# Kernel optimization log

Measured on AMD Instinct MI355X. Metric: run time of the kernel, lower is better.

Reference implementation:

```python
import jax, jax.numpy as jnp
import numpy as np

V = 50000      # word vocab
CV = 63        # char vocab (60 chars + 3 tags)
HW = 512       # word hidden size
HC = 256       # char hidden size
NLW = 2        # word lstm layers
NLC = 2        # char lstm layers
L = 12         # chars in the word


def _lstm_layers(x, H, C, Wih, Whh, bih, bhh):
    """One time-step of a multi-layer LSTM (PyTorch gate order i,f,g,o).
    x: [1, D], H/C: [nl, 1, D]. Returns (top_h, newH, newC)."""
    nl = Wih.shape[0]
    newH, newC = [], []
    inp = x
    for l in range(nl):
        gates = inp @ Wih[l].T + H[l] @ Whh[l].T + bih[l] + bhh[l]  # [1, 4D]
        i, f, g, o = jnp.split(gates, 4, axis=-1)
        i = jax.nn.sigmoid(i)
        f = jax.nn.sigmoid(f)
        g = jnp.tanh(g)
        o = jax.nn.sigmoid(o)
        c = f * C[l] + i * g
        h = o * jnp.tanh(c)
        newH.append(h)
        newC.append(c)
        inp = h
    return inp, jnp.stack(newH), jnp.stack(newC)


def setup_inputs() -> dict:
    key = jax.random.key(0)
    ks = jax.random.split(key, 20)
    sW = 1.0 / np.sqrt(HW)
    sC = 1.0 / np.sqrt(HC)
    return {
        "x_word": jax.random.randint(ks[0], (1,), 0, V),
        "x_char": jax.random.randint(ks[1], (L,), 0, CV),
        "h_word_h": jax.random.normal(ks[2], (NLW, 1, HW), jnp.float32),
        "h_word_c": jax.random.normal(ks[3], (NLW, 1, HW), jnp.float32),
        "h_char_h": jax.random.normal(ks[4], (NLC, 1, HC), jnp.float32),
        "h_char_c": jax.random.normal(ks[5], (NLC, 1, HC), jnp.float32),
        "word_emb": jax.random.normal(ks[6], (V, HW), jnp.float32),
        "word_Wih": jax.random.normal(ks[7], (NLW, 4 * HW, HW), jnp.float32) * sW,
        "word_Whh": jax.random.normal(ks[8], (NLW, 4 * HW, HW), jnp.float32) * sW,
        "word_bih": jax.random.normal(ks[9], (NLW, 4 * HW), jnp.float32) * sW,
        "word_bhh": jax.random.normal(ks[10], (NLW, 4 * HW), jnp.float32) * sW,
        "dec_W": jax.random.normal(ks[11], (V, HW), jnp.float32) * sW,
        "dec_b": jax.random.normal(ks[12], (V,), jnp.float32) * sW,
        "char_emb": jax.random.normal(ks[13], (CV, HC), jnp.float32),
        "char_Wih": jax.random.normal(ks[14], (NLC, 4 * HC, HC), jnp.float32) * sC,
        "char_Whh": jax.random.normal(ks[15], (NLC, 4 * HC, HC), jnp.float32) * sC,
        "char_bih": jax.random.normal(ks[16], (NLC, 4 * HC), jnp.float32) * sC,
        "char_bhh": jax.random.normal(ks[17], (NLC, 4 * HC), jnp.float32) * sC,
        "char_to_embedding": jax.random.normal(ks[18], (HW, HC), jnp.float32),
        "g_w": jax.random.normal(ks[19], (HW,), jnp.float32) * sW,
        "g_b": jax.random.normal(jax.random.fold_in(key, 99), (1,), jnp.float32),
    }


def reference(x_word, x_char, h_word_h, h_word_c, h_char_h, h_char_c,
              word_emb, word_Wih, word_Whh, word_bih, word_bhh,
              dec_W, dec_b,
              char_emb, char_Wih, char_Whh, char_bih, char_bhh,
              char_to_embedding, g_w, g_b):
    # character-level recurrence over the word's characters
    def char_step(carry, cidx):
        H, C = carry
        xc = char_emb[cidx][None, :]  # [1, HC]
        _, H, C = _lstm_layers(xc, H, C, char_Wih, char_Whh, char_bih, char_bhh)
        return (H, C), None

    (h_char_h, h_char_c), _ = jax.lax.scan(char_step, (h_char_h, h_char_c), x_char)

    # note: original uses h_char[1] (the CELL state) of the last layer
    x_c = char_to_embedding @ h_char_c[-1].T          # [HW, 1]
    x_w = word_emb[x_word[0]][None, :]                # [1, HW]
    g = jax.nn.relu(jnp.dot(g_w, x_w[0]) + g_b[0])    # scalar gate
    x = (1.0 - g) * x_w + g * x_c.T                   # [1, HW]

    y, h_word_h, h_word_c = _lstm_layers(x, h_word_h, h_word_c,
                                         word_Wih, word_Whh, word_bih, word_bhh)
    y = y @ dec_W.T + dec_b                           # [1, V]
    return y, h_word_h, h_word_c, h_char_h, h_char_c
```

## Files before the change

### kernel.cpp

```cpp
#include <hip/hip_runtime.h>
#include <stdint.h>


#define SCOPE_AGT __HIP_MEMORY_SCOPE_AGENT
#define ALL64 0xFFFFFFFFFFFFFFFFull

static __device__ __forceinline__ float dot4(float4 w, const float* p){
    return w.x*p[0] + w.y*p[1] + w.z*p[2] + w.w*p[3];
}
static __device__ __forceinline__ float dot44(float4 a, float4 b){
    return a.x*b.x + a.y*b.y + a.z*b.z + a.w*b.w;
}
static __device__ __forceinline__ float sigf(float x){ return 1.0f / (1.0f + __expf(-x)); }
static __device__ __forceinline__ float tanhf_(float x){
    x = fminf(fmaxf(x, -15.0f), 15.0f);
    float e = __expf(2.0f * x);
    return (e - 1.0f) / (e + 1.0f);
}

static __device__ __forceinline__ float gload(const float* p){
    return __hip_atomic_load(p, __ATOMIC_RELAXED, SCOPE_AGT);
}
static __device__ __forceinline__ void gstore(float* p, float v){
    __hip_atomic_store(p, v, __ATOMIC_RELAXED, SCOPE_AGT);
}
static __device__ __forceinline__ int gload_i(const int* p){
    return __hip_atomic_load(p, __ATOMIC_RELAXED, SCOPE_AGT);
}
static __device__ __forceinline__ void gstore_i(int* p, int v){
    __hip_atomic_store(p, v, __ATOMIC_RELAXED, SCOPE_AGT);
}
static __device__ __forceinline__ unsigned long long gload_ll(const float* p){
    return __hip_atomic_load((const unsigned long long*)p, __ATOMIC_RELAXED, SCOPE_AGT);
}
static __device__ __forceinline__ unsigned long long gload_ll_i(const int* p){
    return __hip_atomic_load((const unsigned long long*)p, __ATOMIC_RELAXED, SCOPE_AGT);
}

static __device__ __forceinline__ void dec_prefetch(const float* __restrict__ dec_W,
        int start, int stride, int lane){
    float acc[8] = {0.f,0.f,0.f,0.f,0.f,0.f,0.f,0.f};
    for (int r = start; r < 50000; r += 8*stride){
        #pragma unroll
        for (int k = 0; k < 8; ++k){
            int rr = r + k * stride;
            if (rr < 50000) acc[k] += dec_W[(size_t)rr * 512 + lane * 8];
        }
    }
    float s = acc[0]+acc[1]+acc[2]+acc[3]+acc[4]+acc[5]+acc[6]+acc[7];
    asm volatile("" :: "v"(s));
}

__global__ __launch_bounds__(256, 2) void k_fused(
    const int* __restrict__ x_word, const int* __restrict__ x_char,
    const float* __restrict__ hwh, const float* __restrict__ hwc,
    const float* __restrict__ hch, const float* __restrict__ hcc,
    const float* __restrict__ word_emb,
    const float* __restrict__ wWih, const float* __restrict__ wWhh,
    const float* __restrict__ wbih, const float* __restrict__ wbhh,
    const float* __restrict__ dec_W, const float* __restrict__ dec_b,
    const float* __restrict__ char_emb,
    const float* __restrict__ cWih, const float* __restrict__ cWhh,
    const float* __restrict__ cbih, const float* __restrict__ cbhh,
    const float* __restrict__ cte,
    const float* __restrict__ g_w, const float* __restrict__ g_b,
    float* __restrict__ ws, float* __restrict__ out)
{
    const int tid  = threadIdx.x;
    const int bx   = blockIdx.x;
    const int lane = tid & 63;
    const int wv   = tid >> 6;
    int*   ws_i  = (int*)(ws + 4096);
    int*   seqf  = ws_i;
    int*   w0f   = ws_i + 128;
    int*   w1f   = ws_i + 256;
    int*   cdone = ws_i + 512;
    float* fdata = ws + 4864;

    __shared__ float sHW[512];

    if (bx < 64){
        __shared__ float sH1[256], sH2[256], sE[256], sg1[16], sg2[16];

        const int rg = tid >> 4, lane16 = tid & 15;
        const int gate = rg & 3, uu = rg >> 2;
        const int u = (bx << 2) + uu;
        const int row = (gate << 8) + u, row2 = 1024 + row;

        float4 w1i[4], w1h[4], w2i[4], w2h[4];
        {
            const float4* p1i = (const float4*)(cWih + (size_t)row  * 256) + lane16 * 4;
            const float4* p1h = (const float4*)(cWhh + (size_t)row  * 256) + lane16 * 4;
            const float4* p2i = (const float4*)(cWih + (size_t)row2 * 256) + lane16 * 4;
            const float4* p2h = (const float4*)(cWhh + (size_t)row2 * 256) + lane16 * 4;
            #pragma unroll
            for (int j = 0; j < 4; ++j){ w1i[j]=p1i[j]; w1h[j]=p1h[j]; w2i[j]=p2i[j]; w2h[j]=p2h[j]; }
        }
        const float b1 = cbih[row]  + cbhh[row];
        const float b2 = cbih[row2] + cbhh[row2];

        float c1r = 0.f, c2r = 0.f, h1fin = 0.f, h2fin = 0.f;
        if (tid < 4)      c1r = hcc[(bx<<2) + tid];
        else if (tid < 8) c2r = hcc[256 + (bx<<2) + (tid-4)];

        for (int t = 0; t <= 12; ++t){
            if (t == 0){
                sH1[tid] = hch[tid];
            } else {
                if (t == 1) sH2[tid] = hch[256 + tid];
                if (tid < 64){
                    const int p = (t - 1) & 1;
                    const int* sq = seqf + p*64;
                    while (true){
                        int v = gload_i(sq + tid);
                        if (__ballot(v >= t) == ALL64) break;
                    }
                    const float* dl = fdata + (size_t)(p*64 + tid)*16;
                    union { unsigned long long u; float f[2]; } q0,q1,q2,q3;
                    q0.u = gload_ll(dl + 0);
                    q1.u = gload_ll(dl + 2);
                    q2.u = gload_ll(dl + 4);
                    q3.u = gload_ll(dl + 6);
                    sH1[4*tid+0] = q0.f[0]; sH1[4*tid+1] = q0.f[1];
                    sH1[4*tid+2] = q1.f[0]; sH1[4*tid+3] = q1.f[1];
                    if (t >= 2){
                        sH2[4*tid+0] = q2.f[0]; sH2[4*tid+1] = q2.f[1];
                        sH2[4*tid+2] = q3.f[0]; sH2[4*tid+3] = q3.f[1];
                    }
                }
            }
            if (t < 12) sE[tid] = char_emb[x_char[t]*256 + tid];
            __syncthreads();

            float a1 = 0.f, a2 = 0.f;
            if (t < 12){
                const float* xp = sE  + lane16*16;
                const float* hp = sH1 + lane16*16;
                #pragma unroll
                for (int j = 0; j < 4; ++j) a1 += dot4(w1i[j], xp + 4*j) + dot4(w1h[j], hp + 4*j);
            }
            if (t >= 1){
                const float* xp = sH1 + lane16*16;
                const float* hp = sH2 + lane16*16;
                #pragma unroll
                for (int j = 0; j < 4; ++j) a2 += dot4(w2i[j], xp + 4*j) + dot4(w2h[j], hp + 4*j);
            }
            #pragma unroll
            for (int m = 8; m >= 1; m >>= 1){
                a1 += __shfl_xor(a1, m, 64);
                a2 += __shfl_xor(a2, m, 64);
            }
            if (lane16 == 0){
                if (t < 12) sg1[rg] = a1 + b1;
                if (t >= 1) sg2[rg] = a2 + b2;
            }
            __syncthreads();

            const int p2 = t & 1;
            float* dst = fdata + (size_t)(p2*64 + bx)*16;
            if (tid < 4){
                if (t < 12){
                    float gi = sigf(sg1[tid*4+0]);
                    float gf = sigf(sg1[tid*4+1]);
                    float gg = tanhf_(sg1[tid*4+2]);
                    float go = sigf(sg1[tid*4+3]);
                    float c = gf * c1r + gi * gg;
                    c1r = c;
                    float h = go * tanhf_(c);
                    h1fin = h;
                    gstore(dst + tid, h);
                }
            } else if (tid < 8){
                if (t >= 1){
                    int q = tid - 4;
                    float gi = sigf(sg2[q*4+0]);
                    float gf = sigf(sg2[q*4+1]);
                    float gg = tanhf_(sg2[q*4+2]);
                    float go = sigf(sg2[q*4+3]);
                    float c = gf * c2r + gi * gg;
                    c2r = c;
                    float h = go * tanhf_(c);
                    h2fin = h;
                    if (t < 12) gstore(dst + 4 + q, h);
                    else        gstore(ws + 1280 + (bx<<2) + q, c);
                }
            }
            __syncthreads();
            if (tid == 0) gstore_i(seqf + p2*64 + bx, t + 1);
        }

        if (tid < 4){
            int uh = (bx << 2) + tid;
            out[52048 + uh] = h1fin;
            out[52560 + uh] = c1r;
        } else if (tid < 8){
            int uh = (bx << 2) + (tid - 4);
            out[52048 + 256 + uh] = h2fin;
            out[52560 + 256 + uh] = c2r;
        }

        if (bx == 0 && tid < 64){
            while (true){
                int v = gload_i(seqf + tid);
                if (__ballot(v >= 13) == ALL64) break;
            }
            if (tid == 0) gstore_i(cdone, 1);
        }

    } else if (bx < 192){
        __shared__ float sC2[256];
        __shared__ float sXCW[512];
        __shared__ float sMisc[8];
        const int vw = ((bx - 64) << 2) + wv;
        float4 wi0[4], wi1[4], wh0[4], wh1[4]; float bs[4];
        #pragma unroll
        for (int gq = 0; gq < 4; ++gq){
            const size_t rf = (size_t)((gq << 9) + vw);
            const float4* pi = (const float4*)(wWih + rf*512) + lane*2;
            const float4* ph = (const float4*)(wWhh + rf*512) + lane*2;
            wi0[gq] = pi[0]; wi1[gq] = pi[1];
            wh0[gq] = ph[0]; wh1[gq] = ph[1];
            bs[gq] = wbih[rf] + wbhh[rf];
        }
        const float4* hv = (const float4*)(hwh) + lane*2;
        const float4 hva = hv[0], hvb = hv[1];
        const size_t wbase = (size_t)x_word[0] * 512;
        const float4* wep = (const float4*)(word_emb + wbase) + lane*2;
        const float4 wea = wep[0], web = wep[1];

        if (bx == 64){
            float p = g_w[2*tid]   * word_emb[wbase + 2*tid]
                    + g_w[2*tid+1] * word_emb[wbase + 2*tid+1];
            #pragma unroll
            for (int m = 32; m >= 1; m >>= 1) p += __shfl_xor(p, m, 64);
            if (lane == 0) sMisc[wv] = p;
            __syncthreads();
            if (tid == 0)
                gstore(ws + 3072, fmaxf(sMisc[0]+sMisc[1]+sMisc[2]+sMisc[3] + g_b[0], 0.0f));
        }

        dec_prefetch(dec_W, ((bx - 64) << 2) + wv, 1024, lane);

        if (tid == 0){ while (gload_i(cdone) < 1) __builtin_amdgcn_s_sleep(8); }
        __syncthreads();
        sC2[tid] = gload(ws + 1280 + tid);
        __syncthreads();

        {
            float4 cv  = ((const float4*)(cte + (size_t)vw*256))[lane];
            float4 c2v = ((const float4*)sC2)[lane];
            float acc = dot44(cv, c2v);
            #pragma unroll
            for (int m = 32; m >= 1; m >>= 1) acc += __shfl_xor(acc, m, 64);
            if (lane == 0) gstore(ws + 1536 + vw, acc);
        }
        __syncthreads();
        if (tid == 0) gstore_i(w0f + (bx - 64), 1);
        if (tid < 64){
            while (true){
                unsigned long long v = gload_ll_i(w0f + 2*tid);
                int lo = (int)(v & 0xffffffffu), hi = (int)(v >> 32);
                if (__ballot(lo >= 1 && hi >= 1) == ALL64) break;
            }
        }
        __syncthreads();
        sXCW[tid]       = gload(ws + 1536 + tid);
        sXCW[256 + tid] = gload(ws + 1536 + 256 + tid);
        if (tid == 0) sMisc[4] = gload(ws + 3072);
        __syncthreads();

        {
            const float g  = sMisc[4];
            const float og = 1.0f - g;
            const float4 x0 = ((const float4*)sXCW)[lane*2];
            const float4 x1 = ((const float4*)sXCW)[lane*2 + 1];
            float4 xa, xb;
            xa.x = og*wea.x + g*x0.x; xa.y = og*wea.y + g*x0.y;
            xa.z = og*wea.z + g*x0.z; xa.w = og*wea.w + g*x0.w;
            xb.x = og*web.x + g*x1.x; xb.y = og*web.y + g*x1.y;
            xb.z = og*web.z + g*x1.z; xb.w = og*web.w + g*x1.w;
            float ac[4];
            #pragma unroll
            for (int gq = 0; gq < 4; ++gq){
                float a = dot44(wi0[gq], xa) + dot44(wi1[gq], xb)
                        + dot44(wh0[gq], hva) + dot44(wh1[gq], hvb);
                #pragma unroll
                for (int m = 32; m >= 1; m >>= 1) a += __shfl_xor(a, m, 64);
                ac[gq] = a;
            }
            if (lane == 0){
                float gi = sigf(ac[0] + bs[0]);
                float gf = sigf(ac[1] + bs[1]);
                float gg = tanhf_(ac[2] + bs[2]);
                float go = sigf(ac[3] + bs[3]);
                float c = gf * hwc[vw] + gi * gg;
                float h = go * tanhf_(c);
                gstore(ws + 2048 + vw, h);
                out[50000 + vw] = h;
                out[51024 + vw] = c;
            }
        }
        __syncthreads();
        if (tid == 0) gstore_i(w0f + (bx - 64), 2);

    } else {
        __shared__ float sX1[512];
        const int vw = ((bx - 192) << 2) + wv;
        float4 wi0[4], wi1[4], wh0[4], wh1[4]; float bs[4];
        #pragma unroll
        for (int gq = 0; gq < 4; ++gq){
            const size_t rf = (size_t)(2048 + (gq << 9) + vw);
            const float4* pi = (const float4*)(wWih + rf*512) + lane*2;
            const float4* ph = (const float4*)(wWhh + rf*512) + lane*2;
            wi0[gq] = pi[0]; wi1[gq] = pi[1];
            wh0[gq] = ph[0]; wh1[gq] = ph[1];
            bs[gq] = wbih[rf] + wbhh[rf];
        }
        const float4* hv = (const float4*)(hwh + 512) + lane*2;
        const float4 hva = hv[0], hvb = hv[1];

        dec_prefetch(dec_W, 512 + ((bx - 192) << 2) + wv, 1024, lane);

        if (tid < 64){
            while (true){
                unsigned long long v = gload_ll_i(w0f + 2*tid);
                int lo = (int)(v & 0xffffffffu), hi = (int)(v >> 32);
                if (__ballot(lo >= 2 && hi >= 2) == ALL64) break;
                __builtin_amdgcn_s_sleep(2);
            }
        }
        __syncthreads();
        sX1[tid]       = gload(ws + 2048 + tid);
        sX1[256 + tid] = gload(ws + 2048 + 256 + tid);
        __syncthreads();
        {
            const float4 xa = ((const float4*)sX1)[lane*2];
            const float4 xb = ((const float4*)sX1)[lane*2 + 1];
            float ac[4];
            #pragma unroll
            for (int gq = 0; gq < 4; ++gq){
                float a = dot44(wi0[gq], xa) + dot44(wi1[gq], xb)
                        + dot44(wh0[gq], hva) + dot44(wh1[gq], hvb);
                #pragma unroll
                for (int m = 32; m >= 1; m >>= 1) a += __shfl_xor(a, m, 64);
                ac[gq] = a;
            }
            if (lane == 0){
                float gi = sigf(ac[0] + bs[0]);
                float gf = sigf(ac[1] + bs[1]);
                float gg = tanhf_(ac[2] + bs[2]);
                float go = sigf(ac[3] + bs[3]);
                float c = gf * hwc[512 + vw] + gi * gg;
                float h = go * tanhf_(c);
                gstore(ws + 2560 + vw, h);
                out[50000 + 512 + vw] = h;
                out[51024 + 512 + vw] = c;
            }
        }
        __syncthreads();
        if (tid == 0) gstore_i(w1f + (bx - 192), 1);
    }

    if (tid < 64){
        while (true){
            unsigned long long v = gload_ll_i(w1f + 2*tid);
            int lo = (int)(v & 0xffffffffu), hi = (int)(v >> 32);
            if (__ballot(lo >= 1 && hi >= 1) == ALL64) break;
            __builtin_amdgcn_s_sleep(4);
        }
    }
    __syncthreads();
    sHW[tid]       = gload(ws + 2560 + tid);
    sHW[256 + tid] = gload(ws + 2560 + 256 + tid);
    __syncthreads();
    {
        const int wid = (bx << 2) + wv;
        const int rr = lane >> 3, cc = lane & 7;
        const float4* hq = (const float4*)sHW + cc*16;
        for (int gb = wid; gb < 6250; gb += 1280){
            const int r = gb*8 + rr;
            const float4* wp = (const float4*)(dec_W + (size_t)r*512 + cc*64);
            float4 wbuf[8];
            float acc = 0.f;
            #pragma unroll
            for (int j = 0; j < 8; ++j) wbuf[j] = wp[j];
            #pragma unroll
            for (int j = 0; j < 8; ++j) acc += dot44(wbuf[j], hq[j]);
            #pragma unroll
            for (int j = 0; j < 8; ++j) wbuf[j] = wp[8 + j];
            #pragma unroll
            for (int j = 0; j < 8; ++j) acc += dot44(wbuf[j], hq[8 + j]);
            acc += __shfl_xor(acc, 1, 64);
            acc += __shfl_xor(acc, 2, 64);
            acc += __shfl_xor(acc, 4, 64);
            if (cc == 0) out[r] = acc + dec_b[r];
        }
    }
}

extern "C" void kernel_launch(void* const* d_in, const int* in_sizes, int n_in,
                              void* d_out, int out_size, void* d_ws, size_t ws_size,
                              hipStream_t stream)
{
    const int*   x_word   = (const int*)d_in[0];
    const int*   x_char   = (const int*)d_in[1];
    const float* hwh      = (const float*)d_in[2];
    const float* hwc      = (const float*)d_in[3];
    const float* hch      = (const float*)d_in[4];
    const float* hcc      = (const float*)d_in[5];
    const float* word_emb = (const float*)d_in[6];
    const float* wWih     = (const float*)d_in[7];
    const float* wWhh     = (const float*)d_in[8];
    const float* wbih     = (const float*)d_in[9];
    const float* wbhh     = (const float*)d_in[10];
    const float* dec_W    = (const float*)d_in[11];
    const float* dec_b    = (const float*)d_in[12];
    const float* char_emb = (const float*)d_in[13];
    const float* cWih     = (const float*)d_in[14];
    const float* cWhh     = (const float*)d_in[15];
    const float* cbih     = (const float*)d_in[16];
    const float* cbhh     = (const float*)d_in[17];
    const float* cte      = (const float*)d_in[18];
    const float* g_w      = (const float*)d_in[19];
    const float* g_b      = (const float*)d_in[20];

    float* ws  = (float*)d_ws;
    float* out = (float*)d_out;

    hipMemsetAsync((void*)((char*)d_ws + 16384), 0, 16384, stream);

    hipLaunchKernelGGL(k_fused, dim3(320), dim3(256), 0, stream,
        x_word, x_char, hwh, hwc, hch, hcc, word_emb,
        wWih, wWhh, wbih, wbhh, dec_W, dec_b,
        char_emb, cWih, cWhh, cbih, cbhh, cte, g_w, g_b,
        ws, out);
}
```

Baseline: 306.2 us.

## Embed sequence tags in char-LSTM data, drop dec_W prefetch, restructure decoder GEMV

Each char-LSTM hidden value is now stored as a (value, step) pair with one 64-bit store, so consumers poll the data itself instead of a separate sequence flag. This removes a flag store, a barrier and a dependent load on every recurrent step. The completion signal is spread over 64 separate cache lines, and the dec_W L2 prefetch passes in the middle blocks are removed. The decoder GEMV now has each half-wave handle one row with coalesced float4 loads and the h vector held in registers. Dropping the prefetch means dec_W is no longer warmed in L2 during the recurrence, and the polling loops now reread more data per check.

```diff
diff --git a/kernel.cpp b/kernel.cpp
--- a/kernel.cpp
+++ b/kernel.cpp
@@ -33,23 +33,11 @@
 static __device__ __forceinline__ unsigned long long gload_ll(const float* p){
     return __hip_atomic_load((const unsigned long long*)p, __ATOMIC_RELAXED, SCOPE_AGT);
 }
-static __device__ __forceinline__ unsigned long long gload_ll_i(const int* p){
-    return __hip_atomic_load((const unsigned long long*)p, __ATOMIC_RELAXED, SCOPE_AGT);
-}
-
-static __device__ __forceinline__ void dec_prefetch(const float* __restrict__ dec_W,
-        int start, int stride, int lane){
-    float acc[8] = {0.f,0.f,0.f,0.f,0.f,0.f,0.f,0.f};
-    for (int r = start; r < 50000; r += 8*stride){
-        #pragma unroll
-        for (int k = 0; k < 8; ++k){
-            int rr = r + k * stride;
-            if (rr < 50000) acc[k] += dec_W[(size_t)rr * 512 + lane * 8];
-        }
-    }
-    float s = acc[0]+acc[1]+acc[2]+acc[3]+acc[4]+acc[5]+acc[6]+acc[7];
-    asm volatile("" :: "v"(s));
-}
+static __device__ __forceinline__ void gstore_ll(float* p, unsigned long long v){
+    __hip_atomic_store((unsigned long long*)p, v, __ATOMIC_RELAXED, SCOPE_AGT);
+}
+
+union PairU { unsigned long long u; float f[2]; };
 
 __global__ __launch_bounds__(256, 2) void k_fused(
     const int* __restrict__ x_word, const int* __restrict__ x_char,
@@ -71,11 +59,10 @@
     const int lane = tid & 63;
     const int wv   = tid >> 6;
     int*   ws_i  = (int*)(ws + 4096);
-    int*   seqf  = ws_i;
-    int*   w0f   = ws_i + 128;
-    int*   w1f   = ws_i + 256;
-    int*   cdone = ws_i + 512;
-    float* fdata = ws + 4864;
+    int*   w0f   = ws_i;
+    int*   w1f   = ws_i + 128;
+    int*   cdone = ws_i + 256;
+    float* fdata = ws + 6400;
 
     __shared__ float sHW[512];
 
@@ -110,22 +97,39 @@
                 if (t == 1) sH2[tid] = hch[256 + tid];
                 if (tid < 64){
                     const int p = (t - 1) & 1;
-                    const int* sq = seqf + p*64;
-                    while (true){
-                        int v = gload_i(sq + tid);
-                        if (__ballot(v >= t) == ALL64) break;
-                    }
-                    const float* dl = fdata + (size_t)(p*64 + tid)*16;
-                    union { unsigned long long u; float f[2]; } q0,q1,q2,q3;
-                    q0.u = gload_ll(dl + 0);
-                    q1.u = gload_ll(dl + 2);
-                    q2.u = gload_ll(dl + 4);
-                    q3.u = gload_ll(dl + 6);
-                    sH1[4*tid+0] = q0.f[0]; sH1[4*tid+1] = q0.f[1];
-                    sH1[4*tid+2] = q1.f[0]; sH1[4*tid+3] = q1.f[1];
+                    const float* base = fdata + (size_t)(p*64 + tid)*32;
+                    const float ft = (float)t;
                     if (t >= 2){
-                        sH2[4*tid+0] = q2.f[0]; sH2[4*tid+1] = q2.f[1];
-                        sH2[4*tid+2] = q3.f[0]; sH2[4*tid+3] = q3.f[1];
+                        while (true){
+                            PairU q[8];
+                            #pragma unroll
+                            for (int k = 0; k < 8; ++k) q[k].u = gload_ll(base + 2*k);
+                            bool ok = true;
+                            #pragma unroll
+                            for (int k = 0; k < 8; ++k) ok &= (q[k].f[1] == ft);
+                            if (__ballot(ok) == ALL64){
+                                #pragma unroll
+                                for (int k = 0; k < 4; ++k){
+                                    sH1[4*tid + k] = q[k].f[0];
+                                    sH2[4*tid + k] = q[4+k].f[0];
+                                }
+                                break;
+                            }
+                        }
+                    } else {
+                        while (true){
+                            PairU q[4];
+                            #pragma unroll
+                            for (int k = 0; k < 4; ++k) q[k].u = gload_ll(base + 2*k);
+                            bool ok = true;
+                            #pragma unroll
+                            for (int k = 0; k < 4; ++k) ok &= (q[k].f[1] == ft);
+                            if (__ballot(ok) == ALL64){
+                                #pragma unroll
+                                for (int k = 0; k < 4; ++k) sH1[4*tid + k] = q[k].f[0];
+                                break;
+                            }
+                        }
                     }
                 }
             }
@@ -156,8 +160,7 @@
             }
             __syncthreads();
 
-            const int p2 = t & 1;
-            float* dst = fdata + (size_t)(p2*64 + bx)*16;
+            float* dst = fdata + (size_t)((t & 1)*64 + bx)*32;
             if (tid < 4){
                 if (t < 12){
                     float gi = sigf(sg1[tid*4+0]);
@@ -168,7 +171,8 @@
                     c1r = c;
                     float h = go * tanhf_(c);
                     h1fin = h;
-                    gstore(dst + tid, h);
+                    PairU pr; pr.f[0] = h; pr.f[1] = (float)(t+1);
+                    gstore_ll(dst + 2*tid, pr.u);
                 }
             } else if (tid < 8){
                 if (t >= 1){
@@ -181,12 +185,12 @@
                     c2r = c;
                     float h = go * tanhf_(c);
                     h2fin = h;
-                    if (t < 12) gstore(dst + 4 + q, h);
-                    else        gstore(ws + 1280 + (bx<<2) + q, c);
+                    PairU pr; pr.f[0] = (t < 12) ? h : c;
+                    pr.f[1] = (float)(t+1);
+                    gstore_ll(dst + 8 + 2*q, pr.u);
                 }
             }
             __syncthreads();
-            if (tid == 0) gstore_i(seqf + p2*64 + bx, t + 1);
         }
 
         if (tid < 4){
@@ -200,11 +204,17 @@
         }
 
         if (bx == 0 && tid < 64){
+            const float* base = fdata + (size_t)tid*32;
             while (true){
-                int v = gload_i(seqf + tid);
-                if (__ballot(v >= 13) == ALL64) break;
-            }
-            if (tid == 0) gstore_i(cdone, 1);
+                PairU q[4];
+                #pragma unroll
+                for (int k = 0; k < 4; ++k) q[k].u = gload_ll(base + 8 + 2*k);
+                bool ok = true;
+                #pragma unroll
+                for (int k = 0; k < 4; ++k) ok &= (q[k].f[1] == 13.0f);
+                if (__ballot(ok) == ALL64) break;
+            }
+            gstore_i(cdone + tid*32, 1);
         }
 
     } else if (bx < 192){
@@ -239,11 +249,16 @@
                 gstore(ws + 3072, fmaxf(sMisc[0]+sMisc[1]+sMisc[2]+sMisc[3] + g_b[0], 0.0f));
         }
 
-        dec_prefetch(dec_W, ((bx - 64) << 2) + wv, 1024, lane);
-
-        if (tid == 0){ while (gload_i(cdone) < 1) __builtin_amdgcn_s_sleep(8); }
-        __syncthreads();
-        sC2[tid] = gload(ws + 1280 + tid);
+        if (tid == 0){
+            int* myline = cdone + ((bx - 64) & 63)*32;
+            while (gload_i(myline) < 1) __builtin_amdgcn_s_sleep(4);
+        }
+        __syncthreads();
+        {
+            PairU q;
+            q.u = gload_ll(fdata + (size_t)(tid >> 2)*32 + 8 + 2*(tid & 3));
+            sC2[tid] = q.f[0];
+        }
         __syncthreads();
 
         {
@@ -258,7 +273,7 @@
         if (tid == 0) gstore_i(w0f + (bx - 64), 1);
         if (tid < 64){
             while (true){
-                unsigned long long v = gload_ll_i(w0f + 2*tid);
+                unsigned long long v = gload_ll((const float*)(w0f + 2*tid));
                 int lo = (int)(v & 0xffffffffu), hi = (int)(v >> 32);
                 if (__ballot(lo >= 1 && hi >= 1) == ALL64) break;
             }
@@ -319,11 +334,9 @@
         const float4* hv = (const float4*)(hwh + 512) + lane*2;
         const float4 hva = hv[0], hvb = hv[1];
 
-        dec_prefetch(dec_W, 512 + ((bx - 192) << 2) + wv, 1024, lane);
-
         if (tid < 64){
             while (true){
-                unsigned long long v = gload_ll_i(w0f + 2*tid);
+                unsigned long long v = gload_ll((const float*)(w0f + 2*tid));
                 int lo = (int)(v & 0xffffffffu), hi = (int)(v >> 32);
                 if (__ballot(lo >= 2 && hi >= 2) == ALL64) break;
                 __builtin_amdgcn_s_sleep(2);
@@ -363,10 +376,10 @@
 
     if (tid < 64){
         while (true){
-            unsigned long long v = gload_ll_i(w1f + 2*tid);
+            unsigned long long v = gload_ll((const float*)(w1f + 2*tid));
             int lo = (int)(v & 0xffffffffu), hi = (int)(v >> 32);
             if (__ballot(lo >= 1 && hi >= 1) == ALL64) break;
-            __builtin_amdgcn_s_sleep(4);
+            __builtin_amdgcn_s_sleep(8);
         }
     }
     __syncthreads();
@@ -374,25 +387,28 @@
     sHW[256 + tid] = gload(ws + 2560 + 256 + tid);
     __syncthreads();
     {
-        const int wid = (bx << 2) + wv;
-        const int rr = lane >> 3, cc = lane & 7;
-        const float4* hq = (const float4*)sHW + cc*16;
-        for (int gb = wid; gb < 6250; gb += 1280){
-            const int r = gb*8 + rr;
-            const float4* wp = (const float4*)(dec_W + (size_t)r*512 + cc*64);
-            float4 wbuf[8];
+        const int wid  = (bx << 2) + wv;
+        const int cc   = lane & 31;
+        const int half = lane >> 5;
+        float4 hq[4];
+        const float4* sf4 = (const float4*)sHW;
+        #pragma unroll
+        for (int j = 0; j < 4; ++j) hq[j] = sf4[cc + j*32];
+
+        for (int r0 = wid*2; r0 < 50000; r0 += 2560){
+            const int r = r0 + half;
+            const float4* wp = (const float4*)(dec_W + (size_t)r*512) + cc;
+            float4 wb[4];
+            #pragma unroll
+            for (int j = 0; j < 4; ++j) wb[j] = wp[j*32];
             float acc = 0.f;
             #pragma unroll
-            for (int j = 0; j < 8; ++j) wbuf[j] = wp[j];
-            #pragma unroll
-            for (int j = 0; j < 8; ++j) acc += dot44(wbuf[j], hq[j]);
-            #pragma unroll
-            for (int j = 0; j < 8; ++j) wbuf[j] = wp[8 + j];
-            #pragma unroll
-            for (int j = 0; j < 8; ++j) acc += dot44(wbuf[j], hq[8 + j]);
+            for (int j = 0; j < 4; ++j) acc += dot44(wb[j], hq[j]);
             acc += __shfl_xor(acc, 1, 64);
             acc += __shfl_xor(acc, 2, 64);
             acc += __shfl_xor(acc, 4, 64);
+            acc += __shfl_xor(acc, 8, 64);
+            acc += __shfl_xor(acc, 16, 64);
             if (cc == 0) out[r] = acc + dec_b[r];
         }
     }
@@ -427,7 +443,7 @@
     float* ws  = (float*)d_ws;
     float* out = (float*)d_out;
 
-    hipMemsetAsync((void*)((char*)d_ws + 16384), 0, 16384, stream);
+    hipMemsetAsync((void*)((char*)d_ws + 16384), 0, 32768, stream);
 
     hipLaunchKernelGGL(k_fused, dim3(320), dim3(256), 0, stream,
         x_word, x_char, hwh, hwc, hch, hcc, word_emb,
```

Measured after the change: 299.4 us. -2.2%, faster.
